# Kernel tuning notes

Hardware: AMD Instinct MI355X
Metric: run time of the kernel (lower is better)

## Reference

```python
import jax, jax.numpy as jnp
import numpy as np

N = 1_000_000   # total points across all frames in batch
B = 8           # frames (segments) per batch
C = 256         # bottleneck / backbone_out_channels
H = 512         # lstm_hidden_channels
NUM_CLASSES = 20


def setup_inputs() -> dict:
    key = jax.random.key(0)
    ks = jax.random.split(key, 10)
    s = lambda k, shape, scale=0.02: jax.random.normal(k, shape, dtype=jnp.float32) * scale
    feat = jax.random.normal(ks[0], (N, C), dtype=jnp.float32)
    # cumulative offsets: equal-size segments ending at N (torch offset convention)
    offset = (jnp.arange(1, B + 1, dtype=jnp.int32) * (N // B)).astype(jnp.int32)
    return {
        "feat": feat,
        "offset": offset,
        "W_ih": s(ks[1], (4 * H, C)),
        "b_ih": s(ks[2], (4 * H,)),
        "W_hh": s(ks[3], (4 * H, H)),
        "b_hh": s(ks[4], (4 * H,)),
        "W_proj": s(ks[5], (C, H)),
        "b_proj": s(ks[6], (C,)),
        "W_head": s(ks[7], (NUM_CLASSES, C)),
        "b_head": s(ks[8], (NUM_CLASSES,)),
    }


def reference(feat, offset, W_ih, b_ih, W_hh, b_hh, W_proj, b_proj, W_head, b_head):
    n = feat.shape[0]
    # --- ragged per-segment mean pooling (replaces Python loop over offsets) ---
    seg_id = jnp.searchsorted(offset, jnp.arange(n, dtype=offset.dtype), side="right")
    counts = offset - jnp.concatenate([jnp.zeros((1,), offset.dtype), offset[:-1]])
    sums = jax.ops.segment_sum(feat, seg_id, num_segments=offset.shape[0])  # [B, C]
    pooled = sums / counts[:, None].astype(feat.dtype)                      # [B, C]
    # --- LSTMCell with zero initial (h, c): torch gate order i, f, g, o ---
    gates = pooled @ W_ih.T + b_ih + b_hh                                   # h0 = 0 -> W_hh term drops
    i, f, g, o = jnp.split(gates, 4, axis=-1)
    c = jax.nn.sigmoid(i) * jnp.tanh(g)                                     # f * c0 = 0
    h = jax.nn.sigmoid(o) * jnp.tanh(c)                                     # [B, H]
    _ = jax.nn.sigmoid(f)  # f gate unused with zero cell state (kept implicit)
    # --- temporal projection + broadcast fuse (dropout p=0 in eval) ---
    ctx = h @ W_proj.T + b_proj                                             # [B, C]
    fused = feat + ctx[seg_id]                                              # [N, C]
    # --- segmentation head ---
    seg_logits = fused @ W_head.T + b_head                                  # [N, num_classes]
    return seg_logits
```

## Files before the change

kernel.cpp:

```cpp
#include <hip/hip_runtime.h>
#include <math.h>

#define CDIM 256
#define HDIM 512
#define KCLS 20
#define MAXSEG 8
#define TILE_R 64
#define NTHR 512
#define F4_TILE (TILE_R * CDIM / 4)
#define F4_THR (F4_TILE / NTHR)

__global__ __launch_bounds__(NTHR, 4) void fused_pool_head_kernel(
    const float* __restrict__ feat, const int* __restrict__ offset,
    const float* __restrict__ W_head, const float* __restrict__ b_head,
    float* __restrict__ sums, float* __restrict__ out, int n, int nseg) {
  __shared__ float tile[TILE_R * CDIM];
  float4* tile4 = (float4*)tile;
  int t = threadIdx.x;
  int lane = t & 63;
  int wv = t >> 6;

  int kb_ = (wv < 4) ? wv * 3 : 12 + (wv - 4) * 2;
  int kb = __builtin_amdgcn_readfirstlane(kb_);
  float bh0 = b_head[kb], bh1 = b_head[kb + 1];
  float bh2 = (wv < 4) ? b_head[kb + 2] : 0.f;

  int ntiles = (n + TILE_R - 1) / TILE_R;
  int nb = (int)gridDim.x;
  int t0 = (int)blockIdx.x;

  int off[MAXSEG];
#pragma unroll
  for (int q = 0; q < MAXSEG; ++q) off[q] = (q < nseg) ? offset[q] : 0x7fffffff;

  int col = t & 255;
  int rhalf = (t >> 8) * 32;
  int c4s = col >> 2, js = col & 3;
  float colacc = 0.f;
  int cur_seg = -1;

  const float4* src = (const float4*)feat;
  long lim = (long)n * (CDIM / 4);
  float4 stg[F4_THR];

  if (t0 < ntiles) {
    long base = (long)t0 * F4_TILE;
    if (base + F4_TILE <= lim) {
#pragma unroll
      for (int i = 0; i < F4_THR; ++i) stg[i] = src[base + i * NTHR + t];
    } else {
#pragma unroll
      for (int i = 0; i < F4_THR; ++i) {
        long idx = base + i * NTHR + t;
        stg[i] = (idx < lim) ? src[idx] : make_float4(0.f, 0.f, 0.f, 0.f);
      }
    }
#pragma unroll
    for (int i = 0; i < F4_THR; ++i) {
      int idx = i * NTHR + t;
      int rr = idx >> 6, c4 = idx & 63;
      tile4[rr * 64 + (c4 ^ (rr & 7))] = stg[i];
    }
  }
  __syncthreads();

  for (int tl = t0; tl < ntiles; tl += nb) {
    int nxt = tl + nb;
    bool havenext = (nxt < ntiles);
    long r0 = (long)tl * TILE_R;
    int rows = (int)(((long)n - r0) < TILE_R ? ((long)n - r0) : TILE_R);

    if (havenext) {
      long base = (long)nxt * F4_TILE;
      if (base + F4_TILE <= lim) {
#pragma unroll
        for (int i = 0; i < F4_THR; ++i) stg[i] = src[base + i * NTHR + t];
      } else {
#pragma unroll
        for (int i = 0; i < F4_THR; ++i) {
          long idx = base + i * NTHR + t;
          stg[i] = (idx < lim) ? src[idx] : make_float4(0.f, 0.f, 0.f, 0.f);
        }
      }
    }

    {
      int rlo = rhalf, rhi = rhalf + 32;
      if (rhi > rows) rhi = rows;
      if (rlo < rhi) {
        long ra = r0 + rlo, rb = r0 + rhi - 1;
        int s0 = 0, s1 = 0;
#pragma unroll
        for (int q = 0; q < MAXSEG - 1; ++q) {
          s0 += (ra >= off[q]) ? 1 : 0;
          s1 += (rb >= off[q]) ? 1 : 0;
        }
        if (s0 == s1) {
          if (s0 != cur_seg) {
            if (cur_seg >= 0) atomicAdd(&sums[cur_seg * CDIM + col], colacc);
            colacc = 0.f;
            cur_seg = s0;
          }
          float a = 0.f;
#pragma unroll 8
          for (int rr = rlo; rr < rhi; ++rr)
            a += tile[(rr * 64 + (c4s ^ (rr & 7))) * 4 + js];
          colacc += a;
        } else {
          for (int rr = rlo; rr < rhi; ++rr) {
            long r = r0 + rr;
            int s = 0;
#pragma unroll
            for (int q = 0; q < MAXSEG - 1; ++q) s += (r >= off[q]) ? 1 : 0;
            if (s != cur_seg) {
              if (cur_seg >= 0) atomicAdd(&sums[cur_seg * CDIM + col], colacc);
              colacc = 0.f;
              cur_seg = s;
            }
            colacc += tile[(rr * 64 + (c4s ^ (rr & 7))) * 4 + js];
          }
        }
      }
    }

    if (lane < rows) {
      const float4* trow = tile4 + lane * 64;
      int l7 = lane & 7;
      if (wv < 4) {
        float a0 = bh0, a1 = bh1, a2 = bh2;
        const float* w0 = W_head + (kb + 0) * CDIM;
        const float* w1 = W_head + (kb + 1) * CDIM;
        const float* w2 = W_head + (kb + 2) * CDIM;
#pragma unroll 8
        for (int c4 = 0; c4 < 64; ++c4) {
          float4 f = trow[c4 ^ l7];
          int cb = c4 * 4;
          a0 = fmaf(f.x, w0[cb], a0); a1 = fmaf(f.x, w1[cb], a1); a2 = fmaf(f.x, w2[cb], a2);
          a0 = fmaf(f.y, w0[cb+1], a0); a1 = fmaf(f.y, w1[cb+1], a1); a2 = fmaf(f.y, w2[cb+1], a2);
          a0 = fmaf(f.z, w0[cb+2], a0); a1 = fmaf(f.z, w1[cb+2], a1); a2 = fmaf(f.z, w2[cb+2], a2);
          a0 = fmaf(f.w, w0[cb+3], a0); a1 = fmaf(f.w, w1[cb+3], a1); a2 = fmaf(f.w, w2[cb+3], a2);
        }
        float* orow = out + (r0 + lane) * KCLS + kb;
        orow[0] = a0; orow[1] = a1; orow[2] = a2;
      } else {
        float a0 = bh0, a1 = bh1;
        const float* w0 = W_head + (kb + 0) * CDIM;
        const float* w1 = W_head + (kb + 1) * CDIM;
#pragma unroll 8
        for (int c4 = 0; c4 < 64; ++c4) {
          float4 f = trow[c4 ^ l7];
          int cb = c4 * 4;
          a0 = fmaf(f.x, w0[cb], a0);   a1 = fmaf(f.x, w1[cb], a1);
          a0 = fmaf(f.y, w0[cb+1], a0); a1 = fmaf(f.y, w1[cb+1], a1);
          a0 = fmaf(f.z, w0[cb+2], a0); a1 = fmaf(f.z, w1[cb+2], a1);
          a0 = fmaf(f.w, w0[cb+3], a0); a1 = fmaf(f.w, w1[cb+3], a1);
        }
        float* orow = out + (r0 + lane) * KCLS + kb;
        orow[0] = a0; orow[1] = a1;
      }
    }
    __syncthreads();

    if (havenext) {
#pragma unroll
      for (int i = 0; i < F4_THR; ++i) {
        int idx = i * NTHR + t;
        int rr = idx >> 6, c4 = idx & 63;
        tile4[rr * 64 + (c4 ^ (rr & 7))] = stg[i];
      }
    }
    __syncthreads();
  }
  if (cur_seg >= 0) atomicAdd(&sums[cur_seg * CDIM + col], colacc);
}

__global__ __launch_bounds__(512) void lstm_ctx_kernel(
    const float* __restrict__ sums, const int* __restrict__ offset,
    const float* __restrict__ W_ih, const float* __restrict__ b_ih,
    const float* __restrict__ b_hh, const float* __restrict__ W_proj,
    const float* __restrict__ b_proj, const float* __restrict__ W_head,
    float* __restrict__ delta) {
  __shared__ float pooled[CDIM];
  __shared__ float hs[HDIM];
  __shared__ float ctx[CDIM];
  int s = blockIdx.x;
  int t = threadIdx.x;
  if (t < CDIM) {
    int prev = (s == 0) ? 0 : offset[s - 1];
    float cnt = (float)(offset[s] - prev);
    pooled[t] = sums[(size_t)s * CDIM + t] / cnt;
  }
  __syncthreads();

  {
    const float* Wi = W_ih + (size_t)(0 * HDIM + t) * CDIM;
    const float* Wg = W_ih + (size_t)(2 * HDIM + t) * CDIM;
    const float* Wo = W_ih + (size_t)(3 * HDIM + t) * CDIM;
    float di = b_ih[0 * HDIM + t] + b_hh[0 * HDIM + t];
    float dg = b_ih[2 * HDIM + t] + b_hh[2 * HDIM + t];
    float dd = b_ih[3 * HDIM + t] + b_hh[3 * HDIM + t];
    for (int c = 0; c < CDIM; ++c) {
      float p = pooled[c];
      di = fmaf(p, Wi[c], di);
      dg = fmaf(p, Wg[c], dg);
      dd = fmaf(p, Wo[c], dd);
    }
    float ig = 1.f / (1.f + expf(-di));
    float gg = tanhf(dg);
    float og = 1.f / (1.f + expf(-dd));
    hs[t] = og * tanhf(ig * gg);
  }
  __syncthreads();

  if (t < CDIM) {
    const float* Wp = W_proj + (size_t)t * HDIM;
    float acc = b_proj[t];
    for (int j = 0; j < HDIM; ++j) acc = fmaf(hs[j], Wp[j], acc);
    ctx[t] = acc;
  }
  __syncthreads();

  if (t < KCLS) {
    const float* Wh = W_head + (size_t)t * CDIM;
    float a = 0.f;
    for (int c = 0; c < CDIM; ++c) a = fmaf(ctx[c], Wh[c], a);
    delta[s * KCLS + t] = a;
  }
}

__global__ __launch_bounds__(256) void add_delta_kernel(
    float* __restrict__ out, const int* __restrict__ offset,
    const float* __restrict__ delta, int n, int nseg) {
  __shared__ float dl[MAXSEG * KCLS];
  int t = threadIdx.x;
  if (t < MAXSEG * KCLS) dl[t] = (t < nseg * KCLS) ? delta[t] : 0.f;
  __syncthreads();

  long e4 = (long)blockIdx.x * 256 + t;
  long tot = (long)n * (KCLS / 4);
  if (e4 >= tot) return;
  long row = e4 / 5;
  int k0 = (int)(e4 - row * 5) * 4;

  int off[MAXSEG];
#pragma unroll
  for (int q = 0; q < MAXSEG; ++q) off[q] = (q < nseg) ? offset[q] : 0x7fffffff;
  int s = 0;
#pragma unroll
  for (int q = 0; q < MAXSEG - 1; ++q) s += (row >= off[q]) ? 1 : 0;
  if (s >= nseg) s = nseg - 1;

  float4 v = ((float4*)out)[e4];
  const float* d = &dl[s * KCLS + k0];
  v.x += d[0]; v.y += d[1]; v.z += d[2]; v.w += d[3];
  ((float4*)out)[e4] = v;
}

extern "C" void kernel_launch(void* const* d_in, const int* in_sizes, int n_in,
                              void* d_out, int out_size, void* d_ws, size_t ws_size,
                              hipStream_t stream) {
  const float* feat   = (const float*)d_in[0];
  const int*   offset = (const int*)d_in[1];
  const float* W_ih   = (const float*)d_in[2];
  const float* b_ih   = (const float*)d_in[3];
  const float* b_hh   = (const float*)d_in[5];
  const float* W_proj = (const float*)d_in[6];
  const float* b_proj = (const float*)d_in[7];
  const float* W_head = (const float*)d_in[8];
  const float* b_head = (const float*)d_in[9];
  float* out = (float*)d_out;

  int n = in_sizes[0] / CDIM;
  int nseg = in_sizes[1];
  if (nseg > MAXSEG) nseg = MAXSEG;

  float* ws    = (float*)d_ws;
  float* sums  = ws;
  float* delta = ws + MAXSEG * CDIM;

  hipMemsetAsync(sums, 0, MAXSEG * CDIM * sizeof(float), stream);
  fused_pool_head_kernel<<<512, NTHR, 0, stream>>>(feat, offset, W_head, b_head,
                                                   sums, out, n, nseg);
  lstm_ctx_kernel<<<nseg, 512, 0, stream>>>(sums, offset, W_ih, b_ih, b_hh,
                                            W_proj, b_proj, W_head, delta);
  long tot4 = (long)n * (KCLS / 4);
  int blocksC = (int)((tot4 + 255) / 256);
  add_delta_kernel<<<blocksC, 256, 0, stream>>>(out, offset, delta, n, nseg);
}
```

Baseline: 425.9 us.

## Double-buffer feature prefetch and split LSTM tail into parallel small kernels

The main pooling/head kernel now keeps two register staging buffers, so the global load for the tile two steps ahead is issued while the current tile is computed. The head dot-product unroll drops from 8 to 4, likely to offset the extra register pressure. The single-block-per-segment LSTM/projection/head kernel is split into three kernels (gates, projection, head delta) spread over many blocks, using float4 loads and wave shuffle reductions. The add-delta pass becomes grid-stride with a fixed grid. Doubling the staging registers may lower occupancy, and the extra launches add overhead.

After: 367.5 us. -13.7%, faster.

```diff
diff --git a/kernel.cpp b/kernel.cpp
--- a/kernel.cpp
+++ b/kernel.cpp
@@ -9,6 +9,7 @@
 #define NTHR 512
 #define F4_TILE (TILE_R * CDIM / 4)
 #define F4_THR (F4_TILE / NTHR)
+#define GRIDA 512
 
 __global__ __launch_bounds__(NTHR, 4) void fused_pool_head_kernel(
     const float* __restrict__ feat, const int* __restrict__ offset,
@@ -41,10 +42,10 @@
 
   const float4* src = (const float4*)feat;
   long lim = (long)n * (CDIM / 4);
-  float4 stg[F4_THR];
-
-  if (t0 < ntiles) {
-    long base = (long)t0 * F4_TILE;
+  float4 stgA[F4_THR], stgB[F4_THR];
+
+  auto issue = [&](float4* stg, int tl) {
+    long base = (long)tl * F4_TILE;
     if (base + F4_TILE <= lim) {
 #pragma unroll
       for (int i = 0; i < F4_THR; ++i) stg[i] = src[base + i * NTHR + t];
@@ -55,70 +56,52 @@
         stg[i] = (idx < lim) ? src[idx] : make_float4(0.f, 0.f, 0.f, 0.f);
       }
     }
+  };
+  auto dswrite = [&](const float4* stg) {
 #pragma unroll
     for (int i = 0; i < F4_THR; ++i) {
       int idx = i * NTHR + t;
       int rr = idx >> 6, c4 = idx & 63;
       tile4[rr * 64 + (c4 ^ (rr & 7))] = stg[i];
     }
-  }
-  __syncthreads();
-
-  for (int tl = t0; tl < ntiles; tl += nb) {
-    int nxt = tl + nb;
-    bool havenext = (nxt < ntiles);
+  };
+  auto compute = [&](int tl) {
     long r0 = (long)tl * TILE_R;
     int rows = (int)(((long)n - r0) < TILE_R ? ((long)n - r0) : TILE_R);
 
-    if (havenext) {
-      long base = (long)nxt * F4_TILE;
-      if (base + F4_TILE <= lim) {
-#pragma unroll
-        for (int i = 0; i < F4_THR; ++i) stg[i] = src[base + i * NTHR + t];
+    int rlo = rhalf, rhi = rhalf + 32;
+    if (rhi > rows) rhi = rows;
+    if (rlo < rhi) {
+      long ra = r0 + rlo, rb = r0 + rhi - 1;
+      int s0 = 0, s1 = 0;
+#pragma unroll
+      for (int q = 0; q < MAXSEG - 1; ++q) {
+        s0 += (ra >= off[q]) ? 1 : 0;
+        s1 += (rb >= off[q]) ? 1 : 0;
+      }
+      if (s0 == s1) {
+        if (s0 != cur_seg) {
+          if (cur_seg >= 0) atomicAdd(&sums[cur_seg * CDIM + col], colacc);
+          colacc = 0.f;
+          cur_seg = s0;
+        }
+        float a = 0.f;
+#pragma unroll 8
+        for (int rr = rlo; rr < rhi; ++rr)
+          a += tile[(rr * 64 + (c4s ^ (rr & 7))) * 4 + js];
+        colacc += a;
       } else {
-#pragma unroll
-        for (int i = 0; i < F4_THR; ++i) {
-          long idx = base + i * NTHR + t;
-          stg[i] = (idx < lim) ? src[idx] : make_float4(0.f, 0.f, 0.f, 0.f);
-        }
-      }
-    }
-
-    {
-      int rlo = rhalf, rhi = rhalf + 32;
-      if (rhi > rows) rhi = rows;
-      if (rlo < rhi) {
-        long ra = r0 + rlo, rb = r0 + rhi - 1;
-        int s0 = 0, s1 = 0;
-#pragma unroll
-        for (int q = 0; q < MAXSEG - 1; ++q) {
-          s0 += (ra >= off[q]) ? 1 : 0;
-          s1 += (rb >= off[q]) ? 1 : 0;
-        }
-        if (s0 == s1) {
-          if (s0 != cur_seg) {
+        for (int rr = rlo; rr < rhi; ++rr) {
+          long r = r0 + rr;
+          int s = 0;
+#pragma unroll
+          for (int q = 0; q < MAXSEG - 1; ++q) s += (r >= off[q]) ? 1 : 0;
+          if (s != cur_seg) {
             if (cur_seg >= 0) atomicAdd(&sums[cur_seg * CDIM + col], colacc);
             colacc = 0.f;
-            cur_seg = s0;
+            cur_seg = s;
           }
-          float a = 0.f;
-#pragma unroll 8
-          for (int rr = rlo; rr < rhi; ++rr)
-            a += tile[(rr * 64 + (c4s ^ (rr & 7))) * 4 + js];
-          colacc += a;
-        } else {
-          for (int rr = rlo; rr < rhi; ++rr) {
-            long r = r0 + rr;
-            int s = 0;
-#pragma unroll
-            for (int q = 0; q < MAXSEG - 1; ++q) s += (r >= off[q]) ? 1 : 0;
-            if (s != cur_seg) {
-              if (cur_seg >= 0) atomicAdd(&sums[cur_seg * CDIM + col], colacc);
-              colacc = 0.f;
-              cur_seg = s;
-            }
-            colacc += tile[(rr * 64 + (c4s ^ (rr & 7))) * 4 + js];
-          }
+          colacc += tile[(rr * 64 + (c4s ^ (rr & 7))) * 4 + js];
         }
       }
     }
@@ -131,7 +114,7 @@
         const float* w0 = W_head + (kb + 0) * CDIM;
         const float* w1 = W_head + (kb + 1) * CDIM;
         const float* w2 = W_head + (kb + 2) * CDIM;
-#pragma unroll 8
+#pragma unroll 4
         for (int c4 = 0; c4 < 64; ++c4) {
           float4 f = trow[c4 ^ l7];
           int cb = c4 * 4;
@@ -146,7 +129,7 @@
         float a0 = bh0, a1 = bh1;
         const float* w0 = W_head + (kb + 0) * CDIM;
         const float* w1 = W_head + (kb + 1) * CDIM;
-#pragma unroll 8
+#pragma unroll 4
         for (int c4 = 0; c4 < 64; ++c4) {
           float4 f = trow[c4 ^ l7];
           int cb = c4 * 4;
@@ -159,73 +142,155 @@
         orow[0] = a0; orow[1] = a1;
       }
     }
+  };
+
+  if (t0 < ntiles) issue(stgA, t0);
+  if (t0 + nb < ntiles) issue(stgB, t0 + nb);
+  if (t0 < ntiles) dswrite(stgA);
+  __syncthreads();
+
+  for (int tl = t0; tl < ntiles; tl += 2 * nb) {
+    int tA2 = tl + 2 * nb;
+    if (tA2 < ntiles) issue(stgA, tA2);
+    compute(tl);
     __syncthreads();
-
-    if (havenext) {
-#pragma unroll
-      for (int i = 0; i < F4_THR; ++i) {
-        int idx = i * NTHR + t;
-        int rr = idx >> 6, c4 = idx & 63;
-        tile4[rr * 64 + (c4 ^ (rr & 7))] = stg[i];
-      }
-    }
+    int tB = tl + nb;
+    if (tB < ntiles) dswrite(stgB);
     __syncthreads();
+    if (tB < ntiles) {
+      int tB2 = tl + 3 * nb;
+      if (tB2 < ntiles) issue(stgB, tB2);
+      compute(tB);
+      __syncthreads();
+      if (tA2 < ntiles) dswrite(stgA);
+      __syncthreads();
+    }
   }
   if (cur_seg >= 0) atomicAdd(&sums[cur_seg * CDIM + col], colacc);
 }
 
-__global__ __launch_bounds__(512) void lstm_ctx_kernel(
+__global__ __launch_bounds__(256) void lstm_h_kernel(
     const float* __restrict__ sums, const int* __restrict__ offset,
     const float* __restrict__ W_ih, const float* __restrict__ b_ih,
-    const float* __restrict__ b_hh, const float* __restrict__ W_proj,
-    const float* __restrict__ b_proj, const float* __restrict__ W_head,
-    float* __restrict__ delta) {
-  __shared__ float pooled[CDIM];
-  __shared__ float hs[HDIM];
-  __shared__ float ctx[CDIM];
-  int s = blockIdx.x;
-  int t = threadIdx.x;
-  if (t < CDIM) {
-    int prev = (s == 0) ? 0 : offset[s - 1];
-    float cnt = (float)(offset[s] - prev);
-    pooled[t] = sums[(size_t)s * CDIM + t] / cnt;
-  }
-  __syncthreads();
-
+    const float* __restrict__ b_hh, float* __restrict__ h, int nseg) {
+  __shared__ float pooled[MAXSEG * CDIM];
+  int t = threadIdx.x;
   {
-    const float* Wi = W_ih + (size_t)(0 * HDIM + t) * CDIM;
-    const float* Wg = W_ih + (size_t)(2 * HDIM + t) * CDIM;
-    const float* Wo = W_ih + (size_t)(3 * HDIM + t) * CDIM;
-    float di = b_ih[0 * HDIM + t] + b_hh[0 * HDIM + t];
-    float dg = b_ih[2 * HDIM + t] + b_hh[2 * HDIM + t];
-    float dd = b_ih[3 * HDIM + t] + b_hh[3 * HDIM + t];
-    for (int c = 0; c < CDIM; ++c) {
-      float p = pooled[c];
-      di = fmaf(p, Wi[c], di);
-      dg = fmaf(p, Wg[c], dg);
-      dd = fmaf(p, Wo[c], dd);
-    }
+    int prev = 0;
+    for (int s = 0; s < MAXSEG; ++s) {
+      int cur = (s < nseg) ? offset[s] : prev;
+      float cnt = (float)(cur - prev);
+      float inv = (cnt > 0.f) ? 1.f / cnt : 0.f;
+      pooled[s * CDIM + t] = sums[s * CDIM + t] * inv;
+      prev = cur;
+    }
+  }
+  __syncthreads();
+
+  int wv = t >> 6, l = t & 63;
+  int j = (int)blockIdx.x * 4 + wv;
+  int s = l >> 3, ch = l & 7;
+
+  const float4* Wi4 = (const float4*)(W_ih + (size_t)(0 * HDIM + j) * CDIM);
+  const float4* Wg4 = (const float4*)(W_ih + (size_t)(2 * HDIM + j) * CDIM);
+  const float4* Wo4 = (const float4*)(W_ih + (size_t)(3 * HDIM + j) * CDIM);
+  const float4* p4 = (const float4*)(pooled + s * CDIM);
+
+  float di = 0.f, dg = 0.f, dd = 0.f;
+#pragma unroll
+  for (int i = 0; i < 8; ++i) {
+    int c4 = ch * 8 + i;
+    float4 p = p4[c4];
+    float4 wi = Wi4[c4], wg = Wg4[c4], wo = Wo4[c4];
+    di = fmaf(p.x, wi.x, di); di = fmaf(p.y, wi.y, di);
+    di = fmaf(p.z, wi.z, di); di = fmaf(p.w, wi.w, di);
+    dg = fmaf(p.x, wg.x, dg); dg = fmaf(p.y, wg.y, dg);
+    dg = fmaf(p.z, wg.z, dg); dg = fmaf(p.w, wg.w, dg);
+    dd = fmaf(p.x, wo.x, dd); dd = fmaf(p.y, wo.y, dd);
+    dd = fmaf(p.z, wo.z, dd); dd = fmaf(p.w, wo.w, dd);
+  }
+#pragma unroll
+  for (int m = 1; m < 8; m <<= 1) {
+    di += __shfl_xor(di, m);
+    dg += __shfl_xor(dg, m);
+    dd += __shfl_xor(dd, m);
+  }
+  if (ch == 0 && s < nseg) {
+    di += b_ih[j] + b_hh[j];
+    dg += b_ih[2 * HDIM + j] + b_hh[2 * HDIM + j];
+    dd += b_ih[3 * HDIM + j] + b_hh[3 * HDIM + j];
     float ig = 1.f / (1.f + expf(-di));
     float gg = tanhf(dg);
     float og = 1.f / (1.f + expf(-dd));
-    hs[t] = og * tanhf(ig * gg);
-  }
-  __syncthreads();
-
-  if (t < CDIM) {
-    const float* Wp = W_proj + (size_t)t * HDIM;
-    float acc = b_proj[t];
-    for (int j = 0; j < HDIM; ++j) acc = fmaf(hs[j], Wp[j], acc);
-    ctx[t] = acc;
-  }
-  __syncthreads();
-
-  if (t < KCLS) {
-    const float* Wh = W_head + (size_t)t * CDIM;
-    float a = 0.f;
-    for (int c = 0; c < CDIM; ++c) a = fmaf(ctx[c], Wh[c], a);
-    delta[s * KCLS + t] = a;
-  }
+    h[(size_t)s * HDIM + j] = og * tanhf(ig * gg);
+  }
+}
+
+__global__ __launch_bounds__(256) void ctx_kernel(
+    const float* __restrict__ h, const float* __restrict__ W_proj,
+    const float* __restrict__ b_proj, float* __restrict__ ctx, int nseg) {
+  __shared__ float hs[MAXSEG * HDIM];
+  int t = threadIdx.x;
+  {
+    const float4* hsrc = (const float4*)h;
+    float4* hdst = (float4*)hs;
+#pragma unroll
+    for (int i = 0; i < 4; ++i) hdst[i * 256 + t] = hsrc[i * 256 + t];
+  }
+  __syncthreads();
+
+  int wv = t >> 6, l = t & 63;
+  int col = (int)blockIdx.x * 4 + wv;
+  int s = l >> 3, ch = l & 7;
+
+  const float4* Wp4 = (const float4*)(W_proj + (size_t)col * HDIM);
+  const float4* h4 = (const float4*)(hs + s * HDIM);
+  float acc = 0.f;
+#pragma unroll
+  for (int i = 0; i < 16; ++i) {
+    int j4 = ch * 16 + i;
+    float4 hv = h4[j4];
+    float4 w = Wp4[j4];
+    acc = fmaf(hv.x, w.x, acc); acc = fmaf(hv.y, w.y, acc);
+    acc = fmaf(hv.z, w.z, acc); acc = fmaf(hv.w, w.w, acc);
+  }
+#pragma unroll
+  for (int m = 1; m < 8; m <<= 1) acc += __shfl_xor(acc, m);
+  if (ch == 0 && s < nseg) ctx[s * CDIM + col] = acc + b_proj[col];
+}
+
+__global__ __launch_bounds__(256) void delta_kernel(
+    const float* __restrict__ ctx, const float* __restrict__ W_head,
+    float* __restrict__ delta, int nseg) {
+  __shared__ float cs[MAXSEG * CDIM];
+  int t = threadIdx.x;
+  {
+    const float4* csrc = (const float4*)ctx;
+    float4* cdst = (float4*)cs;
+#pragma unroll
+    for (int i = 0; i < 2; ++i) cdst[i * 256 + t] = csrc[i * 256 + t];
+  }
+  __syncthreads();
+
+  int wv = t >> 6, l = t & 63;
+  int k = (int)blockIdx.x * 4 + wv;
+  if (k >= KCLS) return;
+  int s = l >> 3, ch = l & 7;
+
+  const float4* Wh4 = (const float4*)(W_head + (size_t)k * CDIM);
+  const float4* c4 = (const float4*)(cs + s * CDIM);
+  float acc = 0.f;
+#pragma unroll
+  for (int i = 0; i < 8; ++i) {
+    int idx = ch * 8 + i;
+    float4 cv = c4[idx];
+    float4 w = Wh4[idx];
+    acc = fmaf(cv.x, w.x, acc); acc = fmaf(cv.y, w.y, acc);
+    acc = fmaf(cv.z, w.z, acc); acc = fmaf(cv.w, w.w, acc);
+  }
+#pragma unroll
+  for (int m = 1; m < 8; m <<= 1) acc += __shfl_xor(acc, m);
+  if (ch == 0 && s < nseg) delta[s * KCLS + k] = acc;
 }
 
 __global__ __launch_bounds__(256) void add_delta_kernel(
@@ -236,24 +301,23 @@
   if (t < MAXSEG * KCLS) dl[t] = (t < nseg * KCLS) ? delta[t] : 0.f;
   __syncthreads();
 
-  long e4 = (long)blockIdx.x * 256 + t;
+  int off[MAXSEG];
+#pragma unroll
+  for (int q = 0; q < MAXSEG; ++q) off[q] = (q < nseg) ? offset[q] : 0x7fffffff;
+
   long tot = (long)n * (KCLS / 4);
-  if (e4 >= tot) return;
-  long row = e4 / 5;
-  int k0 = (int)(e4 - row * 5) * 4;
-
-  int off[MAXSEG];
-#pragma unroll
-  for (int q = 0; q < MAXSEG; ++q) off[q] = (q < nseg) ? offset[q] : 0x7fffffff;
-  int s = 0;
-#pragma unroll
-  for (int q = 0; q < MAXSEG - 1; ++q) s += (row >= off[q]) ? 1 : 0;
-  if (s >= nseg) s = nseg - 1;
-
-  float4 v = ((float4*)out)[e4];
-  const float* d = &dl[s * KCLS + k0];
-  v.x += d[0]; v.y += d[1]; v.z += d[2]; v.w += d[3];
-  ((float4*)out)[e4] = v;
+  long stride = (long)gridDim.x * 256;
+  for (long e4 = (long)blockIdx.x * 256 + t; e4 < tot; e4 += stride) {
+    long row = e4 / 5;
+    int k0 = (int)(e4 - row * 5) * 4;
+    int s = 0;
+#pragma unroll
+    for (int q = 0; q < MAXSEG - 1; ++q) s += (row >= off[q]) ? 1 : 0;
+    float4 v = ((float4*)out)[e4];
+    const float* d = &dl[s * KCLS + k0];
+    v.x += d[0]; v.y += d[1]; v.z += d[2]; v.w += d[3];
+    ((float4*)out)[e4] = v;
+  }
 }
 
 extern "C" void kernel_launch(void* const* d_in, const int* in_sizes, int n_in,
@@ -276,14 +340,15 @@
 
   float* ws    = (float*)d_ws;
   float* sums  = ws;
-  float* delta = ws + MAXSEG * CDIM;
+  float* h     = ws + MAXSEG * CDIM;
+  float* ctx   = ws + MAXSEG * CDIM + MAXSEG * HDIM;
+  float* delta = ctx + MAXSEG * CDIM;
 
   hipMemsetAsync(sums, 0, MAXSEG * CDIM * sizeof(float), stream);
-  fused_pool_head_kernel<<<512, NTHR, 0, stream>>>(feat, offset, W_head, b_head,
-                                                   sums, out, n, nseg);
-  lstm_ctx_kernel<<<nseg, 512, 0, stream>>>(sums, offset, W_ih, b_ih, b_hh,
-                                            W_proj, b_proj, W_head, delta);
-  long tot4 = (long)n * (KCLS / 4);
-  int blocksC = (int)((tot4 + 255) / 256);
-  add_delta_kernel<<<blocksC, 256, 0, stream>>>(out, offset, delta, n, nseg);
-}
+  fused_pool_head_kernel<<<GRIDA, NTHR, 0, stream>>>(feat, offset, W_head, b_head,
+                                                     sums, out, n, nseg);
+  lstm_h_kernel<<<128, 256, 0, stream>>>(sums, offset, W_ih, b_ih, b_hh, h, nseg);
+  ctx_kernel<<<64, 256, 0, stream>>>(h, W_proj, b_proj, ctx, nseg);
+  delta_kernel<<<5, 256, 0, stream>>>(ctx, W_head, delta, nseg);
+  add_delta_kernel<<<2048, 256, 0, stream>>>(out, offset, delta, n, nseg);
+}
```
